# Kernel optimization log

Measured on AMD Instinct MI355X. Metric: run time of the kernel, lower is better.

Reference implementation:

```python
import jax, jax.numpy as jnp
import numpy as np

N, G, L, C = 32768, 128, 256, 128   # nodes, graphs, nodes-per-graph, channels
E, DS, DC, DR = 524288, 16, 4, 8    # edges, d_state, d_conv, dt_rank
EPS = 1e-5


def setup_inputs():
    key = jax.random.key(0)
    ks = jax.random.split(key, 16)
    s = 0.02
    p = lambda i, shape: jax.random.normal(ks[i], shape, jnp.float32) * s
    return {
        "x": jax.random.normal(ks[0], (N, C), jnp.float32),
        "edge_index": jax.random.randint(ks[1], (2, E), 0, N),
        "batch": jnp.repeat(jnp.arange(G), L),  # uniform graph sizes, sorted
        "gin_eps": jnp.float32(0.0),
        "gin_w1": p(2, (C, C)), "gin_b1": jnp.zeros((C,), jnp.float32),
        "gin_w2": p(3, (C, C)), "gin_b2": jnp.zeros((C,), jnp.float32),
        "in_proj_w": p(4, (2 * C, C)),
        "conv_w": p(5, (C, DC)), "conv_b": jnp.zeros((C,), jnp.float32),
        "x_proj_w": p(6, (DR + 2 * DS, C)),
        "dt_proj_w": p(7, (C, DR)),
        "dt_proj_b": jnp.full((C,), -4.0, jnp.float32),  # softplus -> small dt
        "A_log": jnp.log(jnp.broadcast_to(jnp.arange(1, DS + 1, dtype=jnp.float32), (C, DS))),
        "Dp": jnp.ones((C,), jnp.float32),
        "out_proj_w": p(8, (C, C)),
        "mlp_w1": p(9, (2 * C, C)), "mlp_b1": jnp.zeros((2 * C,), jnp.float32),
        "mlp_w2": p(10, (C, 2 * C)), "mlp_b2": jnp.zeros((C,), jnp.float32),
        "g1": jnp.ones((C,), jnp.float32), "be1": jnp.zeros((C,), jnp.float32),
        "g2": jnp.ones((C,), jnp.float32), "be2": jnp.zeros((C,), jnp.float32),
        "g3": jnp.ones((C,), jnp.float32), "be3": jnp.zeros((C,), jnp.float32),
    }


def batch_norm(h, g, b):
    # BatchNorm1d forward (batch statistics, biased var), eps=1e-5
    mu = h.mean(0)
    var = h.var(0)
    return (h - mu) * jax.lax.rsqrt(var + EPS) * g + b


def mamba(xd, in_proj_w, conv_w, conv_b, x_proj_w, dt_proj_w, dt_proj_b, A_log, Dp, out_proj_w):
    # xd: [G, L, C]; Mamba with expand=1 (d_inner == C)
    xz = jnp.einsum('glc,dc->gld', xd, in_proj_w)        # [G,L,2C]
    xs, z = jnp.split(xz, 2, axis=-1)
    # depthwise causal conv1d, kernel DC, left-pad DC-1
    xc = jax.lax.conv_general_dilated(
        xs.transpose(0, 2, 1), conv_w[:, None, :], (1,), [(DC - 1, 0)],
        dimension_numbers=('NCH', 'OIH', 'NCH'), feature_group_count=C)
    xs = jax.nn.silu(xc.transpose(0, 2, 1) + conv_b)     # [G,L,C]
    xdbl = jnp.einsum('gld,ed->gle', xs, x_proj_w)       # [G,L,DR+2*DS]
    dtr, Bm, Cm = jnp.split(xdbl, [DR, DR + DS], axis=-1)
    dt = jax.nn.softplus(jnp.einsum('glr,dr->gld', dtr, dt_proj_w) + dt_proj_b)  # [G,L,C]
    A = -jnp.exp(A_log)                                   # [C,DS]

    def step(hst, t):
        dt_t, B_t, C_t, x_t = t                           # [G,C],[G,DS],[G,DS],[G,C]
        dA = jnp.exp(dt_t[..., None] * A)                 # [G,C,DS]
        hst = dA * hst + dt_t[..., None] * B_t[:, None, :] * x_t[..., None]
        return hst, (hst * C_t[:, None, :]).sum(-1)       # y_t: [G,C]

    h0 = jnp.zeros((G, C, DS), xd.dtype)
    _, y = jax.lax.scan(step, h0, (dt.transpose(1, 0, 2), Bm.transpose(1, 0, 2),
                                   Cm.transpose(1, 0, 2), xs.transpose(1, 0, 2)))
    y = y.transpose(1, 0, 2) + Dp * xs                    # [G,L,C]
    y = y * jax.nn.silu(z)
    return jnp.einsum('gld,cd->glc', y, out_proj_w)


def _forward(edge_index, x, gin_eps, gin_w1, gin_b1, gin_w2, gin_b2,
             in_proj_w, conv_w, conv_b, x_proj_w, dt_proj_w, dt_proj_b,
             A_log, Dp, out_proj_w, mlp_w1, mlp_b1, mlp_w2, mlp_b2,
             g1, be1, g2, be2, g3, be3):
    # --- local MPNN branch: GIN conv + residual + norm1 (dropout=0, eval) ---
    agg = jax.ops.segment_sum(x[edge_index[0]], edge_index[1], num_segments=N)
    hg = (1.0 + gin_eps) * x + agg
    hg = jax.nn.relu(hg @ gin_w1.T + gin_b1) @ gin_w2.T + gin_b2
    h1 = batch_norm(hg + x, g1, be1)
    # --- Mamba branch over dense batch (uniform sizes -> reshape, mask all-true) ---
    xd = x.reshape(G, L, C)
    hm = mamba(xd, in_proj_w, conv_w, conv_b, x_proj_w, dt_proj_w, dt_proj_b,
               A_log, Dp, out_proj_w).reshape(N, C)
    h2 = batch_norm(hm + x, g2, be2)
    # --- combine + MLP + norm3 ---
    out = h1 + h2
    out = out + (jax.nn.relu(out @ mlp_w1.T + mlp_b1) @ mlp_w2.T + mlp_b2)
    out = batch_norm(out, g3, be3)
    return out, h2


def reference(x, edge_index, batch, gin_eps, gin_w1, gin_b1, gin_w2, gin_b2,
              in_proj_w, conv_w, conv_b, x_proj_w, dt_proj_w, dt_proj_b,
              A_log, Dp, out_proj_w, mlp_w1, mlp_b1, mlp_w2, mlp_b2,
              g1, be1, g2, be2, g3, be3):
    del batch  # uniform graph sizes encoded in (G, L)
    return _forward(edge_index, x, gin_eps, gin_w1, gin_b1, gin_w2, gin_b2,
                    in_proj_w, conv_w, conv_b, x_proj_w, dt_proj_w, dt_proj_b,
                    A_log, Dp, out_proj_w, mlp_w1, mlp_b1, mlp_w2, mlp_b2,
                    g1, be1, g2, be2, g3, be3)
```

## Files before the change

kernel.cpp:

```cpp
#include <hip/hip_runtime.h>
#include <hip/hip_bf16.h>

#define NN 32768
#define GG 128
#define LL 256
#define CC 128
#define EE 524288
#define NCHUNK 8
#define TCH 32

typedef __attribute__((ext_vector_type(8))) short short8v;
typedef __attribute__((ext_vector_type(4))) short short4v;
typedef __attribute__((ext_vector_type(4))) float floatx4;

__device__ inline short f2bf(float f) {
    __hip_bfloat16 h = __float2bfloat16(f);
    short s; __builtin_memcpy(&s, &h, 2); return s;
}
__device__ inline float b2f(unsigned short u) {
    unsigned v = ((unsigned)u) << 16; float f; __builtin_memcpy(&f, &v, 4); return f;
}
__device__ inline floatx4 mfma16(short8v a, short8v b, floatx4 c) {
    return __builtin_amdgcn_mfma_f32_16x16x32_bf16(a, b, c, 0, 0, 0);
}
__device__ inline float softplus_f(float v) {
    return (v > 20.f) ? v : __logf(1.f + __expf(v));
}

__global__ __launch_bounds__(256)
void wprep_kernel(const float* __restrict__ gw1, const float* __restrict__ gw2,
                  const float* __restrict__ ipw, const float* __restrict__ xpw,
                  const float* __restrict__ opw, const float* __restrict__ mw1,
                  const float* __restrict__ mw2, const float* __restrict__ dtw,
                  unsigned short* __restrict__ wb, int* __restrict__ cnt,
                  float* __restrict__ stats)
{
    int b = blockIdx.x, tid = threadIdx.x;
    if (b < 74) {
        const float* src; int dstoff, lb;
        if (b < 8)       { src = gw1;        dstoff = 0;      lb = b; }
        else if (b < 16) { src = gw2;        dstoff = 16384;  lb = b - 8; }
        else if (b < 32) { src = ipw;        dstoff = 32768;  lb = b - 16; }
        else if (b < 34) { src = xpw + 1024; dstoff = 81920;  lb = b - 32; }
        else if (b < 42) { src = opw;        dstoff = 86016;  lb = b - 34; }
        else if (b < 58) { src = mw1;        dstoff = 102400; lb = b - 42; }
        else             { src = mw2;        dstoff = 135168; lb = b - 58; }
        size_t i = (size_t)lb * 2048 + tid * 8;
        float4 a = *(const float4*)(src + i);
        float4 c = *(const float4*)(src + i + 4);
        short8v s = { f2bf(a.x), f2bf(a.y), f2bf(a.z), f2bf(a.w),
                      f2bf(c.x), f2bf(c.y), f2bf(c.z), f2bf(c.w) };
        *(short8v*)(wb + dstoff + i) = s;
    } else if (b < 138) {
        int i = (b - 74) * 256 + tid;
        int d = i >> 7, c = i & 127;
        float s = 0.f;
#pragma unroll
        for (int r = 0; r < 8; r++) s = fmaf(dtw[d * 8 + r], xpw[r * 128 + c], s);
        wb[65536 + i] = (unsigned short)f2bf(s);
    } else if (b < 170) {
        int idx = (b - 138) * 1024 + tid * 4;
        *(int4*)(cnt + idx) = make_int4(0, 0, 0, 0);
    } else {
        stats[tid] = 0.f; stats[256 + tid] = 0.f; stats[512 + tid] = 0.f;
    }
}

__global__ __launch_bounds__(256) void hist_kernel(const int* __restrict__ ei,
    int* __restrict__ cnt)
{
    int e = blockIdx.x * 256 + threadIdx.x;
    atomicAdd(&cnt[ei[EE + e]], 1);
}

__global__ __launch_bounds__(1024) void scan32k_kernel(const int* __restrict__ cnt,
    int* __restrict__ base, int* __restrict__ cursor)
{
    __shared__ int part[1024];
    int tid = threadIdx.x;
    int local[32];
    int s = 0;
#pragma unroll
    for (int j = 0; j < 32; j++) { local[j] = cnt[tid * 32 + j]; s += local[j]; }
    part[tid] = s;
    __syncthreads();
    for (int off = 1; off < 1024; off <<= 1) {
        int v = (tid >= off) ? part[tid - off] : 0;
        __syncthreads();
        part[tid] += v;
        __syncthreads();
    }
    int run = part[tid] - s;
#pragma unroll
    for (int j = 0; j < 32; j++) {
        base[tid * 32 + j] = run;
        cursor[tid * 32 + j] = run;
        run += local[j];
    }
    if (tid == 0) base[NN] = EE;
}

__global__ __launch_bounds__(256) void permute_kernel(const int* __restrict__ ei,
    int* __restrict__ cursor, int* __restrict__ perm)
{
    int e = blockIdx.x * 256 + threadIdx.x;
    int dst = ei[EE + e];
    int pos = atomicAdd(&cursor[dst], 1);
    perm[pos] = ei[e];
}

__global__ __launch_bounds__(256) void gather_kernel(const int* __restrict__ perm,
    const int* __restrict__ base, const unsigned short* __restrict__ xb,
    const float* __restrict__ epsp, unsigned short* __restrict__ hgin)
{
    int node = blockIdx.x * 8 + (threadIdx.x >> 5);
    int c4 = threadIdx.x & 31;
    int b0 = base[node], b1 = base[node + 1];
    float s0 = 0, s1 = 0, s2 = 0, s3 = 0;
    float t0 = 0, t1 = 0, t2 = 0, t3 = 0;
    int i = b0;
    for (; i + 1 < b1; i += 2) {
        short4v v0 = *(const short4v*)(xb + (size_t)perm[i] * CC + c4 * 4);
        short4v v1 = *(const short4v*)(xb + (size_t)perm[i + 1] * CC + c4 * 4);
        s0 += b2f((unsigned short)v0[0]); s1 += b2f((unsigned short)v0[1]);
        s2 += b2f((unsigned short)v0[2]); s3 += b2f((unsigned short)v0[3]);
        t0 += b2f((unsigned short)v1[0]); t1 += b2f((unsigned short)v1[1]);
        t2 += b2f((unsigned short)v1[2]); t3 += b2f((unsigned short)v1[3]);
    }
    if (i < b1) {
        short4v v0 = *(const short4v*)(xb + (size_t)perm[i] * CC + c4 * 4);
        s0 += b2f((unsigned short)v0[0]); s1 += b2f((unsigned short)v0[1]);
        s2 += b2f((unsigned short)v0[2]); s3 += b2f((unsigned short)v0[3]);
    }
    float e1 = 1.f + epsp[0];
    short4v xv = *(const short4v*)(xb + (size_t)node * CC + c4 * 4);
    float r0 = fmaf(e1, b2f((unsigned short)xv[0]), s0 + t0);
    float r1 = fmaf(e1, b2f((unsigned short)xv[1]), s1 + t1);
    float r2 = fmaf(e1, b2f((unsigned short)xv[2]), s2 + t2);
    float r3 = fmaf(e1, b2f((unsigned short)xv[3]), s3 + t3);
    short4v o = { f2bf(r0), f2bf(r1), f2bf(r2), f2bf(r3) };
    *(short4v*)(hgin + (size_t)node * CC + c4 * 4) = o;
}

__global__ __launch_bounds__(256) void xb_kernel(const float* __restrict__ x,
    unsigned short* __restrict__ xb)
{
    size_t i = (size_t)blockIdx.x * 256 + threadIdx.x;
    float4 a = *(const float4*)(x + i * 8);
    float4 b = *(const float4*)(x + i * 8 + 4);
    short8v s = { f2bf(a.x), f2bf(a.y), f2bf(a.z), f2bf(a.w),
                  f2bf(b.x), f2bf(b.y), f2bf(b.z), f2bf(b.w) };
    *(short8v*)(xb + i * 8) = s;
}

template<int K, int ACT, bool HAS_BIAS, int RESID, bool STATS, int OUTM>
__global__ __launch_bounds__(256)
void rgemm(const unsigned short* __restrict__ A,
           const unsigned short* __restrict__ Wb,
           const float* __restrict__ bias,
           const unsigned short* __restrict__ residb,
           float* out, float* out_b1,
           unsigned short* outb, unsigned short* outb_b1, int ldo,
           float* ssum, float* ssq)
{
    __shared__ float sred[256];
    const int tid = threadIdx.x;
    const int by = blockIdx.y;
    const int lane = tid & 63;
    const int wc = tid >> 6;
    const int rql = lane & 15;
    const int kseg = (lane >> 4) * 8;
    const int rsub = (lane >> 4) * 4;
    constexpr int NK = K / 32;

    if (STATS) sred[tid] = 0.f;

    int colg[2];
    colg[0] = by * 128 + wc * 32 + rql;
    colg[1] = colg[0] + 16;
    short8v w0[NK], w1[NK];
    {
        const unsigned short* wp0 = Wb + (size_t)colg[0] * K + kseg;
        const unsigned short* wp1 = Wb + (size_t)colg[1] * K + kseg;
#pragma unroll
        for (int kk = 0; kk < NK; kk++) {
            w0[kk] = *(const short8v*)(wp0 + kk * 32);
            w1[kk] = *(const short8v*)(wp1 + kk * 32);
        }
    }
    float bcol[2] = {0.f, 0.f};
    if (HAS_BIAS) { bcol[0] = bias[colg[0]]; bcol[1] = bias[colg[1]]; }
    float ssumr[2] = {0.f, 0.f}, ssqr[2] = {0.f, 0.f};

    short8v abuf[2][NK][2];
    {
        const unsigned short* ap = A + (size_t)(blockIdx.x * 32 + rql) * K + kseg;
#pragma unroll
        for (int kk = 0; kk < NK; kk++) {
            abuf[0][kk][0] = *(const short8v*)(ap + kk * 32);
            abuf[0][kk][1] = *(const short8v*)(ap + 16 * K + kk * 32);
        }
    }
    float* op = by ? out_b1 : out;
    unsigned short* opb = by ? outb_b1 : outb;

#pragma unroll
    for (int t = 0; t < 2; t++) {
        const int R0 = (blockIdx.x + t * 512) * 32;
        if (t == 0) {
            const unsigned short* ap = A + (size_t)((blockIdx.x + 512) * 32 + rql) * K + kseg;
#pragma unroll
            for (int kk = 0; kk < NK; kk++) {
                abuf[1][kk][0] = *(const short8v*)(ap + kk * 32);
                abuf[1][kk][1] = *(const short8v*)(ap + 16 * K + kk * 32);
            }
        }
        __builtin_amdgcn_sched_barrier(0);
        floatx4 acc[2][2];
#pragma unroll
        for (int m = 0; m < 2; m++)
#pragma unroll
            for (int n = 0; n < 2; n++)
#pragma unroll
                for (int r = 0; r < 4; r++) acc[m][n][r] = 0.f;
#pragma unroll
        for (int kk = 0; kk < NK; kk++) {
            acc[0][0] = mfma16(abuf[t][kk][0], w0[kk], acc[0][0]);
            acc[0][1] = mfma16(abuf[t][kk][0], w1[kk], acc[0][1]);
            acc[1][0] = mfma16(abuf[t][kk][1], w0[kk], acc[1][0]);
            acc[1][1] = mfma16(abuf[t][kk][1], w1[kk], acc[1][1]);
        }
#pragma unroll
        for (int m = 0; m < 2; m++) {
#pragma unroll
            for (int r = 0; r < 4; r++) {
                int row_g = R0 + m * 16 + rsub + r;
#pragma unroll
                for (int n = 0; n < 2; n++) {
                    float v = acc[m][n][r] + bcol[n];
                    if (ACT == 1) v = fmaxf(v, 0.f);
                    if (ACT == 2) v = softplus_f(v);
                    if (RESID == 1)
                        v += b2f(residb[(size_t)row_g * CC + colg[n]]);
                    int cl_ = colg[n] - by * 128;
                    if (OUTM & 1) op[(size_t)row_g * ldo + cl_] = v;
                    if (OUTM & 2) opb[(size_t)row_g * ldo + cl_] = (unsigned short)f2bf(v);
                    if (STATS) { ssumr[n] += v; ssqr[n] += v * v; }
                }
            }
        }
    }
    if (STATS) {
        __syncthreads();
#pragma unroll
        for (int n = 0; n < 2; n++) {
            int cl = wc * 32 + n * 16 + rql;
            atomicAdd(&sred[cl], ssumr[n]);
            atomicAdd(&sred[128 + cl], ssqr[n]);
        }
        __syncthreads();
        if (tid < 128) {
            atomicAdd(&ssum[tid], sred[tid]);
            atomicAdd(&ssq[tid], sred[128 + tid]);
        }
    }
}

template<int KMID>
__global__ __launch_bounds__(256)
void fused2(const unsigned short* __restrict__ A,
            const unsigned short* __restrict__ W1b, const float* __restrict__ b1,
            const unsigned short* __restrict__ W2b, const float* __restrict__ b2,
            const unsigned short* __restrict__ residb,
            float* __restrict__ outp,
            float* ssum, float* ssq)
{
    constexpr int NF1 = KMID / 64;
    constexpr int NK1 = 4;
    constexpr int NK2 = KMID / 32;
    constexpr int LDSW = KMID + 8;
    __shared__ unsigned short lds[2][32 * LDSW];
    __shared__ float sred[256];
    const int tid = threadIdx.x;
    const int lane = tid & 63;
    const int wc = tid >> 6;
    const int rql = lane & 15;
    const int kseg = (lane >> 4) * 8;
    const int rsub = (lane >> 4) * 4;

    sred[tid] = 0.f;

    short8v w1r[NF1][NK1];
    int colg1[NF1];
    float b1c[NF1];
#pragma unroll
    for (int f = 0; f < NF1; f++) {
        colg1[f] = wc * (16 * NF1) + f * 16 + rql;
        const unsigned short* wp = W1b + (size_t)colg1[f] * 128 + kseg;
#pragma unroll
        for (int kk = 0; kk < NK1; kk++) w1r[f][kk] = *(const short8v*)(wp + kk * 32);
        b1c[f] = b1[colg1[f]];
    }
    int colg2[2];
    colg2[0] = wc * 32 + rql;
    colg2[1] = colg2[0] + 16;
    float b2c[2] = { b2[colg2[0]], b2[colg2[1]] };
    float ssumr[2] = {0.f, 0.f}, ssqr[2] = {0.f, 0.f};

    short8v abuf[2][NK1][2];
    {
        const unsigned short* ap = A + (size_t)(blockIdx.x * 32 + rql) * 128 + kseg;
#pragma unroll
        for (int kk = 0; kk < NK1; kk++) {
            abuf[0][kk][0] = *(const short8v*)(ap + kk * 32);
            abuf[0][kk][1] = *(const short8v*)(ap + 16 * 128 + kk * 32);
        }
    }
    __syncthreads();

#pragma unroll
    for (int t = 0; t < 2; t++) {
        const int R0 = (blockIdx.x + t * 512) * 32;
        floatx4 acc1[2][NF1];
#pragma unroll
        for (int m = 0; m < 2; m++)
#pragma unroll
            for (int f = 0; f < NF1; f++)
#pragma unroll
                for (int r = 0; r < 4; r++) acc1[m][f][r] = 0.f;
#pragma unroll
        for (int kk = 0; kk < NK1; kk++)
#pragma unroll
            for (int m = 0; m < 2; m++)
#pragma unroll
                for (int f = 0; f < NF1; f++)
                    acc1[m][f] = mfma16(abuf[t][kk][m], w1r[f][kk], acc1[m][f]);
        unsigned short* L = &lds[t][0];
#pragma unroll
        for (int m = 0; m < 2; m++)
#pragma unroll
            for (int f = 0; f < NF1; f++)
#pragma unroll
                for (int r = 0; r < 4; r++) {
                    float v = fmaxf(acc1[m][f][r] + b1c[f], 0.f);
                    L[(m * 16 + rsub + r) * LDSW + colg1[f]] = (unsigned short)f2bf(v);
                }
        __syncthreads();
        if (t == 0) {
            const unsigned short* ap = A + (size_t)((blockIdx.x + 512) * 32 + rql) * 128 + kseg;
#pragma unroll
            for (int kk = 0; kk < NK1; kk++) {
                abuf[1][kk][0] = *(const short8v*)(ap + kk * 32);
                abuf[1][kk][1] = *(const short8v*)(ap + 16 * 128 + kk * 32);
            }
        }
        short8v w2a[NK2], w2b[NK2];
        {
            const unsigned short* wq0 = W2b + (size_t)colg2[0] * KMID + kseg;
            const unsigned short* wq1 = W2b + (size_t)colg2[1] * KMID + kseg;
#pragma unroll
            for (int kk = 0; kk < NK2; kk++) {
                w2a[kk] = *(const short8v*)(wq0 + kk * 32);
                w2b[kk] = *(const short8v*)(wq1 + kk * 32);
            }
        }
        floatx4 acc2[2][2];
#pragma unroll
        for (int m = 0; m < 2; m++)
#pragma unroll
            for (int n = 0; n < 2; n++)
#pragma unroll
                for (int r = 0; r < 4; r++) acc2[m][n][r] = 0.f;
#pragma unroll
        for (int kk = 0; kk < NK2; kk++) {
            short8v a2lo = *(const short8v*)&L[rql * LDSW + kseg + kk * 32];
            short8v a2hi = *(const short8v*)&L[(rql + 16) * LDSW + kseg + kk * 32];
            acc2[0][0] = mfma16(a2lo, w2a[kk], acc2[0][0]);
            acc2[0][1] = mfma16(a2lo, w2b[kk], acc2[0][1]);
            acc2[1][0] = mfma16(a2hi, w2a[kk], acc2[1][0]);
            acc2[1][1] = mfma16(a2hi, w2b[kk], acc2[1][1]);
        }
#pragma unroll
        for (int m = 0; m < 2; m++) {
#pragma unroll
            for (int r = 0; r < 4; r++) {
                int row_g = R0 + m * 16 + rsub + r;
#pragma unroll
                for (int n = 0; n < 2; n++) {
                    float v = acc2[m][n][r] + b2c[n];
                    v += b2f(residb[(size_t)row_g * CC + colg2[n]]);
                    outp[(size_t)row_g * CC + colg2[n]] = v;
                    ssumr[n] += v; ssqr[n] += v * v;
                }
            }
        }
    }
    __syncthreads();
#pragma unroll
    for (int n = 0; n < 2; n++) {
        atomicAdd(&sred[colg2[n]], ssumr[n]);
        atomicAdd(&sred[128 + colg2[n]], ssqr[n]);
    }
    __syncthreads();
    if (tid < 128) {
        atomicAdd(&ssum[tid], sred[tid]);
        atomicAdd(&ssq[tid], sred[128 + tid]);
    }
}

__global__ __launch_bounds__(256)
void mamba_front(const unsigned short* __restrict__ xb,
                 const unsigned short* __restrict__ ipwb,
                 const float* __restrict__ cw, const float* __restrict__ cb,
                 const unsigned short* __restrict__ wdtb, const float* __restrict__ dtbv,
                 const unsigned short* __restrict__ xpwb,
                 unsigned short* __restrict__ xsb, unsigned short* __restrict__ zb,
                 unsigned short* __restrict__ dtout, float* __restrict__ BCout)
{
    __shared__ unsigned short xsL[48 * 136];
    __shared__ unsigned short xcL[32 * 136];
    const int tid = threadIdx.x;
    const int lane = tid & 63;
    const int wv = tid >> 6;
    const int rql = lane & 15;
    const int kseg = (lane >> 4) * 8;
    const int rsub = (lane >> 4) * 4;
    const int R0 = blockIdx.x * 32;
    const int RB = R0 - 16;

    int coln[4];
#pragma unroll
    for (int n = 0; n < 4; n++) coln[n] = wv * 64 + n * 16 + rql;
    short8v wr[4][4];
#pragma unroll
    for (int n = 0; n < 4; n++) {
        const unsigned short* wp = ipwb + (size_t)coln[n] * 128 + kseg;
#pragma unroll
        for (int kk = 0; kk < 4; kk++) wr[n][kk] = *(const short8v*)(wp + kk * 32);
    }
    int arow[3];
#pragma unroll
    for (int m = 0; m < 3; m++) {
        int r = RB + m * 16 + rql;
        arow[m] = r < 0 ? 0 : r;
    }
    floatx4 acc[3][4];
#pragma unroll
    for (int m = 0; m < 3; m++)
#pragma unroll
        for (int n = 0; n < 4; n++)
#pragma unroll
            for (int r = 0; r < 4; r++) acc[m][n][r] = 0.f;
#pragma unroll
    for (int kb = 0; kb < 4; kb += 2) {
        short8v a2[3][2];
#pragma unroll
        for (int m = 0; m < 3; m++)
#pragma unroll
            for (int j = 0; j < 2; j++)
                a2[m][j] = *(const short8v*)(xb + (size_t)arow[m] * 128 + kseg + (kb + j) * 32);
        __builtin_amdgcn_sched_barrier(0);
#pragma unroll
        for (int j = 0; j < 2; j++)
#pragma unroll
            for (int m = 0; m < 3; m++)
#pragma unroll
                for (int n = 0; n < 4; n++)
                    acc[m][n] = mfma16(a2[m][j], wr[n][kb + j], acc[m][n]);
    }
    if (wv < 2) {
#pragma unroll
        for (int m = 0; m < 3; m++)
#pragma unroll
            for (int r = 0; r < 4; r++) {
                int row_l = m * 16 + rsub + r;
#pragma unroll
                for (int n = 0; n < 4; n++)
                    xsL[row_l * 136 + coln[n]] = (unsigned short)f2bf(acc[m][n][r]);
            }
    } else {
#pragma unroll
        for (int m = 1; m < 3; m++)
#pragma unroll
            for (int r = 0; r < 4; r++) {
                int row_g = RB + m * 16 + rsub + r;
#pragma unroll
                for (int n = 0; n < 4; n++)
                    zb[(size_t)row_g * 128 + (coln[n] - 128)] = (unsigned short)f2bf(acc[m][n][r]);
            }
    }
    __syncthreads();

    {
        int r = tid >> 3;
        int c0 = (tid & 7) * 16;
        int l = (R0 + r) & (LL - 1);
        const unsigned short* basep = &xsL[(16 + r) * 136 + c0];
        unsigned short o16[16];
#pragma unroll
        for (int half = 0; half < 2; half++) {
            short8v x0 = *(const short8v*)(basep + half * 8);
            short8v x1 = *(const short8v*)(basep - 136 + half * 8);
            short8v x2 = *(const short8v*)(basep - 272 + half * 8);
            short8v x3 = *(const short8v*)(basep - 408 + half * 8);
#pragma unroll
            for (int j = 0; j < 8; j++) {
                int c = c0 + half * 8 + j;
                float4 w = *(const float4*)(cw + c * 4);
                float v = cb[c];
                v = fmaf(b2f((unsigned short)x0[j]), w.w, v);
                if (l >= 1) v = fmaf(b2f((unsigned short)x1[j]), w.z, v);
                if (l >= 2) v = fmaf(b2f((unsigned short)x2[j]), w.y, v);
                if (l >= 3) v = fmaf(b2f((unsigned short)x3[j]), w.x, v);
                v = v / (1.f + __expf(-v));
                o16[half * 8 + j] = (unsigned short)f2bf(v);
            }
        }
#pragma unroll
        for (int half = 0; half < 2; half++) {
            short8v s;
#pragma unroll
            for (int j = 0; j < 8; j++) s[j] = (short)o16[half * 8 + j];
            *(short8v*)&xcL[r * 136 + c0 + half * 8] = s;
            *(short8v*)(xsb + (size_t)(R0 + r) * 128 + c0 + half * 8) = s;
        }
    }
    __syncthreads();

    int cold0 = wv * 32 + rql, cold1 = cold0 + 16;
    short8v wd0[4], wd1[4];
    {
        const unsigned short* wp0 = wdtb + (size_t)cold0 * 128 + kseg;
        const unsigned short* wp1 = wdtb + (size_t)cold1 * 128 + kseg;
#pragma unroll
        for (int kk = 0; kk < 4; kk++) {
            wd0[kk] = *(const short8v*)(wp0 + kk * 32);
            wd1[kk] = *(const short8v*)(wp1 + kk * 32);
        }
    }
    float bd0 = dtbv[cold0], bd1 = dtbv[cold1];
    int colb = wv * 16 + rql;
    short8v wbc[4];
    if (wv < 2) {
        const unsigned short* wp = xpwb + (size_t)colb * 128 + kseg;
#pragma unroll
        for (int kk = 0; kk < 4; kk++) wbc[kk] = *(const short8v*)(wp + kk * 32);
    }
    short8v a0[4], a1[4];
#pragma unroll
    for (int kk = 0; kk < 4; kk++) {
        a0[kk] = *(const short8v*)&xcL[rql * 136 + kseg + kk * 32];
        a1[kk] = *(const short8v*)&xcL[(16 + rql) * 136 + kseg + kk * 32];
    }
    floatx4 accd[2][2], accb[2];
#pragma unroll
    for (int m = 0; m < 2; m++) {
#pragma unroll
        for (int n = 0; n < 2; n++)
#pragma unroll
            for (int r = 0; r < 4; r++) accd[m][n][r] = 0.f;
#pragma unroll
        for (int r = 0; r < 4; r++) accb[m][r] = 0.f;
    }
#pragma unroll
    for (int kk = 0; kk < 4; kk++) {
        accd[0][0] = mfma16(a0[kk], wd0[kk], accd[0][0]);
        accd[0][1] = mfma16(a0[kk], wd1[kk], accd[0][1]);
        accd[1][0] = mfma16(a1[kk], wd0[kk], accd[1][0]);
        accd[1][1] = mfma16(a1[kk], wd1[kk], accd[1][1]);
        if (wv < 2) {
            accb[0] = mfma16(a0[kk], wbc[kk], accb[0]);
            accb[1] = mfma16(a1[kk], wbc[kk], accb[1]);
        }
    }
#pragma unroll
    for (int m = 0; m < 2; m++) {
#pragma unroll
        for (int r = 0; r < 4; r++) {
            int row_g = R0 + m * 16 + rsub + r;
            float v0 = softplus_f(accd[m][0][r] + bd0);
            float v1 = softplus_f(accd[m][1][r] + bd1);
            dtout[(size_t)row_g * 128 + cold0] = (unsigned short)f2bf(v0);
            dtout[(size_t)row_g * 128 + cold1] = (unsigned short)f2bf(v1);
            if (wv < 2) BCout[(size_t)row_g * 32 + colb] = accb[m][r];
        }
    }
}

__global__ __launch_bounds__(256) void scan_part_kernel(const float* __restrict__ BCp,
    const unsigned short* __restrict__ dtp, const unsigned short* __restrict__ xsp_,
    const float* __restrict__ Alog, float* __restrict__ Q, float* __restrict__ SDT)
{
    __shared__ float Bs[TCH * 16];
    __shared__ float dts[TCH * 64];
    __shared__ float xss[TCH * 64];
    int b = blockIdx.x;
    int g = b >> 4, ch = (b >> 3) & 1, chunk = b & 7;
    int t0 = chunk * TCH;
    int tid = threadIdx.x;
    for (int i4 = tid; i4 < TCH * 4; i4 += 256) {
        int t = i4 >> 2, j4 = i4 & 3;
        *(float4*)&Bs[t * 16 + j4 * 4] =
            *(const float4*)(BCp + (size_t)(g * LL + t0 + t) * 32 + j4 * 4);
    }
    for (int i4 = tid; i4 < TCH * 16; i4 += 256) {
        int t = i4 >> 4, c4 = i4 & 15;
        size_t off = (size_t)(g * LL + t0 + t) * CC + ch * 64 + c4 * 4;
        short4v dv = *(const short4v*)(dtp + off);
        short4v xv = *(const short4v*)(xsp_ + off);
        *(float4*)&dts[t * 64 + c4 * 4] = make_float4(
            b2f((unsigned short)dv[0]), b2f((unsigned short)dv[1]),
            b2f((unsigned short)dv[2]), b2f((unsigned short)dv[3]));
        *(float4*)&xss[t * 64 + c4 * 4] = make_float4(
            b2f((unsigned short)xv[0]), b2f((unsigned short)xv[1]),
            b2f((unsigned short)xv[2]), b2f((unsigned short)xv[3]));
    }
    int cl = tid >> 2, sp = tid & 3;
    int c = ch * 64 + cl;
    float ae[4];
#pragma unroll
    for (int j = 0; j < 4; j++) ae[j] = -__expf(Alog[c * 16 + sp * 4 + j]);
    __syncthreads();
    float q0 = 0, q1 = 0, q2 = 0, q3 = 0, sdt = 0;
    for (int t = TCH - 1; t >= 0; --t) {
        float dtv = dts[t * 64 + cl];
        float xv  = xss[t * 64 + cl];
        float u = dtv * xv;
        const float* bs = Bs + t * 16 + sp * 4;
        q0 = fmaf(__expf(ae[0] * sdt) * u, bs[0], q0);
        q1 = fmaf(__expf(ae[1] * sdt) * u, bs[1], q1);
        q2 = fmaf(__expf(ae[2] * sdt) * u, bs[2], q2);
        q3 = fmaf(__expf(ae[3] * sdt) * u, bs[3], q3);
        sdt += dtv;
    }
    float4* qp = (float4*)(Q + (((size_t)g * NCHUNK + chunk) * CC + c) * 16 + sp * 4);
    *qp = make_float4(q0, q1, q2, q3);
    if (sp == 0) SDT[((size_t)g * NCHUNK + chunk) * CC + c] = sdt;
}

__global__ __launch_bounds__(256) void scan_combine_kernel(const float* __restrict__ Q,
    const float* __restrict__ SDT, const float* __restrict__ Alog, float* __restrict__ Hin)
{
    int idx = blockIdx.x * 256 + threadIdx.x;
    int g = idx >> 11;
    int cs = idx & 2047;
    float ae = -__expf(Alog[cs]);
    float h = 0.f;
#pragma unroll
    for (int k = 0; k < NCHUNK; k++) {
        size_t o = ((size_t)g * NCHUNK + k);
        Hin[o * 2048 + cs] = h;
        float sdt = SDT[o * CC + (cs >> 4)];
        h = fmaf(__expf(ae * sdt), h, Q[o * 2048 + cs]);
    }
}

__global__ __launch_bounds__(256) void scan_final_kernel(const float* __restrict__ BCp,
    const unsigned short* __restrict__ dtp, const unsigned short* __restrict__ xsp_,
    const unsigned short* __restrict__ zb, const float* __restrict__ Alog,
    const float* __restrict__ Dp, const float* __restrict__ Hin,
    unsigned short* __restrict__ y2b)
{
    __shared__ float BCs[TCH * 32];
    __shared__ float dts[TCH * 64];
    __shared__ float xss[TCH * 64];
    int b = blockIdx.x;
    int g = b >> 4, ch = (b >> 3) & 1, chunk = b & 7;
    int t0 = chunk * TCH;
    int tid = threadIdx.x;
    for (int i4 = tid; i4 < TCH * 8; i4 += 256) {
        int t = i4 >> 3, j4 = i4 & 7;
        *(float4*)&BCs[t * 32 + j4 * 4] =
            *(const float4*)(BCp + (size_t)(g * LL + t0 + t) * 32 + j4 * 4);
    }
    for (int i4 = tid; i4 < TCH * 16; i4 += 256) {
        int t = i4 >> 4, c4 = i4 & 15;
        size_t off = (size_t)(g * LL + t0 + t) * CC + ch * 64 + c4 * 4;
        short4v dv = *(const short4v*)(dtp + off);
        short4v xv = *(const short4v*)(xsp_ + off);
        *(float4*)&dts[t * 64 + c4 * 4] = make_float4(
            b2f((unsigned short)dv[0]), b2f((unsigned short)dv[1]),
            b2f((unsigned short)dv[2]), b2f((unsigned short)dv[3]));
        *(float4*)&xss[t * 64 + c4 * 4] = make_float4(
            b2f((unsigned short)xv[0]), b2f((unsigned short)xv[1]),
            b2f((unsigned short)xv[2]), b2f((unsigned short)xv[3]));
    }
    int cl = tid >> 2, sp = tid & 3;
    int c = ch * 64 + cl;
    float ae[4];
#pragma unroll
    for (int j = 0; j < 4; j++) ae[j] = -__expf(Alog[c * 16 + sp * 4 + j]);
    float dpc = Dp[c];
    float4 hv = *(const float4*)(Hin + ((size_t)g * NCHUNK + chunk) * 2048 + c * 16 + sp * 4);
    float h0 = hv.x, h1 = hv.y, h2 = hv.z, h3 = hv.w;
    __syncthreads();
    const unsigned short* zg = zb + (size_t)(g * LL + t0) * CC + c;
    unsigned short* yg = y2b + (size_t)(g * LL + t0) * CC + c;
    for (int t = 0; t < TCH; t++) {
        float dtv = dts[t * 64 + cl];
        float xv  = xss[t * 64 + cl];
        float u = dtv * xv;
        const float* bc = BCs + t * 32 + sp * 4;
        h0 = fmaf(__expf(dtv * ae[0]), h0, u * bc[0]);
        h1 = fmaf(__expf(dtv * ae[1]), h1, u * bc[1]);
        h2 = fmaf(__expf(dtv * ae[2]), h2, u * bc[2]);
        h3 = fmaf(__expf(dtv * ae[3]), h3, u * bc[3]);
        float y = h0 * bc[16] + h1 * bc[17] + h2 * bc[18] + h3 * bc[19];
        y += __shfl_xor(y, 1);
        y += __shfl_xor(y, 2);
        if (sp == 0) {
            float zv = b2f(zg[t * CC]);
            float yo = fmaf(dpc, xv, y);
            yg[t * CC] = (unsigned short)f2bf(yo * (zv / (1.f + __expf(-zv))));
        }
    }
}

__global__ __launch_bounds__(256) void norm12_kernel(const float* __restrict__ p1,
    const float* __restrict__ p2, const float* __restrict__ stats,
    const float* g1, const float* be1, const float* g2, const float* be2,
    float* __restrict__ h2out, unsigned short* __restrict__ out12b)
{
    __shared__ float sc[512];
    int tid = threadIdx.x;
    if (tid < 128) {
        int c = tid;
        const float inv = 1.0f / NN;
        float m1 = stats[c] * inv;
        float v1 = fmaxf(stats[128 + c] * inv - m1 * m1, 0.f);
        float i1 = rsqrtf(v1 + 1e-5f);
        sc[c] = g1[c] * i1; sc[128 + c] = be1[c] - m1 * g1[c] * i1;
        float m2 = stats[256 + c] * inv;
        float v2 = fmaxf(stats[384 + c] * inv - m2 * m2, 0.f);
        float i2 = rsqrtf(v2 + 1e-5f);
        sc[256 + c] = g2[c] * i2; sc[384 + c] = be2[c] - m2 * g2[c] * i2;
    }
    __syncthreads();
    size_t idx = (size_t)blockIdx.x * 256 + tid;
    int c4 = (int)(idx & 31);
    float4 s1 = *(float4*)&sc[c4 * 4];
    float4 t1 = *(float4*)&sc[128 + c4 * 4];
    float4 s2 = *(float4*)&sc[256 + c4 * 4];
    float4 t2 = *(float4*)&sc[384 + c4 * 4];
    float4 a = *(const float4*)(p1 + idx * 4);
    float4 b = *(const float4*)(p2 + idx * 4);
    float4 h, o;
    h.x = fmaf(b.x, s2.x, t2.x); o.x = fmaf(a.x, s1.x, t1.x) + h.x;
    h.y = fmaf(b.y, s2.y, t2.y); o.y = fmaf(a.y, s1.y, t1.y) + h.y;
    h.z = fmaf(b.z, s2.z, t2.z); o.z = fmaf(a.z, s1.z, t1.z) + h.z;
    h.w = fmaf(b.w, s2.w, t2.w); o.w = fmaf(a.w, s1.w, t1.w) + h.w;
    *(float4*)(h2out + idx * 4) = h;
    short4v ob = { f2bf(o.x), f2bf(o.y), f2bf(o.z), f2bf(o.w) };
    *(short4v*)(out12b + idx * 4) = ob;
}

__global__ __launch_bounds__(256) void norm3_kernel(const float* __restrict__ p3,
    const float* __restrict__ stats, const float* g3, const float* be3,
    float* __restrict__ outp)
{
    __shared__ float sc[256];
    int tid = threadIdx.x;
    if (tid < 128) {
        int c = tid;
        const float inv = 1.0f / NN;
        float m = stats[512 + c] * inv;
        float v = fmaxf(stats[640 + c] * inv - m * m, 0.f);
        float iv = rsqrtf(v + 1e-5f);
        sc[c] = g3[c] * iv; sc[128 + c] = be3[c] - m * g3[c] * iv;
    }
    __syncthreads();
    size_t idx = (size_t)blockIdx.x * 256 + tid;
    int c4 = (int)(idx & 31);
    float4 s = *(float4*)&sc[c4 * 4];
    float4 t = *(float4*)&sc[128 + c4 * 4];
    float4 a = *(const float4*)(p3 + idx * 4);
    float4 o;
    o.x = fmaf(a.x, s.x, t.x); o.y = fmaf(a.y, s.y, t.y);
    o.z = fmaf(a.z, s.z, t.z); o.w = fmaf(a.w, s.w, t.w);
    *(float4*)(outp + idx * 4) = o;
}

extern "C" void kernel_launch(void* const* d_in, const int* in_sizes, int n_in,
                              void* d_out, int out_size, void* d_ws, size_t ws_size,
                              hipStream_t stream)
{
    (void)in_sizes; (void)n_in; (void)out_size; (void)ws_size;
    const float* x    = (const float*)d_in[0];
    const int*   ei   = (const int*)d_in[1];
    const float* eps  = (const float*)d_in[3];
    const float* gw1  = (const float*)d_in[4];
    const float* gb1  = (const float*)d_in[5];
    const float* gw2  = (const float*)d_in[6];
    const float* gb2  = (const float*)d_in[7];
    const float* ipw  = (const float*)d_in[8];
    const float* cw   = (const float*)d_in[9];
    const float* cb   = (const float*)d_in[10];
    const float* xpw  = (const float*)d_in[11];
    const float* dtw  = (const float*)d_in[12];
    const float* dtb  = (const float*)d_in[13];
    const float* Alog = (const float*)d_in[14];
    const float* Dp   = (const float*)d_in[15];
    const float* opw  = (const float*)d_in[16];
    const float* mw1  = (const float*)d_in[17];
    const float* mb1  = (const float*)d_in[18];
    const float* mw2  = (const float*)d_in[19];
    const float* mb2  = (const float*)d_in[20];
    const float* g1   = (const float*)d_in[21];
    const float* be1  = (const float*)d_in[22];
    const float* g2   = (const float*)d_in[23];
    const float* be2  = (const float*)d_in[24];
    const float* g3   = (const float*)d_in[25];
    const float* be3  = (const float*)d_in[26];

    float* outp = (float*)d_out;
    float* h2o  = outp + (size_t)NN * CC;
    float* p1 = outp;
    float* p2 = h2o;

    const size_t M1 = 1u << 20;
    float* ws = (float*)d_ws;
    float*  scr4   = ws;
    float*  BC     = ws + 4 * M1;
    unsigned short* zb      = (unsigned short*)(ws + 7 * M1);
    unsigned short* dtb_buf = (unsigned short*)(ws + 9 * M1);
    unsigned short* xb      = (unsigned short*)(ws + 11 * M1);
    unsigned short* hgin    = (unsigned short*)(ws + 13 * M1);
    unsigned short* xsb     = (unsigned short*)(ws + 15 * M1);
    unsigned short* out12b  = (unsigned short*)(ws + 17 * M1);
    float*  stats  = ws + 19 * M1;
    int*    cnt    = (int*)(stats + 768);
    int*    baseA  = cnt + NN;
    int*    cursor = baseA + NN + 1;
    int*    perm   = cursor + NN;
    float*  SDT    = (float*)(perm + EE);
    unsigned short* wbase = (unsigned short*)(SDT + 131072);
    unsigned short* gw1b = wbase;
    unsigned short* gw2b = wbase + 16384;
    unsigned short* ipwb = wbase + 32768;
    unsigned short* wdtb = wbase + 65536;
    unsigned short* xpwb = wbase + 81920;
    unsigned short* opwb = wbase + 86016;
    unsigned short* mw1b = wbase + 102400;
    unsigned short* mw2b = wbase + 135168;

    float* Qbuf = scr4;
    float* Hin  = scr4 + 2 * M1;
    float* p3   = scr4;
    unsigned short* y2b = hgin;

    wprep_kernel<<<dim3(171), 256, 0, stream>>>(gw1, gw2, ipw, xpw, opw, mw1, mw2,
                                                dtw, wbase, cnt, stats);
    xb_kernel<<<dim3(NN * CC / 8 / 256), 256, 0, stream>>>(x, xb);

    hist_kernel<<<dim3(EE / 256), 256, 0, stream>>>(ei, cnt);
    scan32k_kernel<<<dim3(1), 1024, 0, stream>>>(cnt, baseA, cursor);
    permute_kernel<<<dim3(EE / 256), 256, 0, stream>>>(ei, cursor, perm);
    gather_kernel<<<dim3(NN / 8), 256, 0, stream>>>(perm, baseA, xb, eps, hgin);

    fused2<128><<<dim3(512), 256, 0, stream>>>(
        hgin, gw1b, gb1, gw2b, gb2, xb, p1, stats + 0, stats + 128);

    mamba_front<<<dim3(NN / 32), 256, 0, stream>>>(
        xb, ipwb, cw, cb, wdtb, dtb, xpwb, xsb, zb, dtb_buf, BC);

    scan_part_kernel<<<dim3(GG * 16), 256, 0, stream>>>(BC, dtb_buf, xsb, Alog, Qbuf, SDT);
    scan_combine_kernel<<<dim3(GG * 2048 / 256), 256, 0, stream>>>(Qbuf, SDT, Alog, Hin);
    scan_final_kernel<<<dim3(GG * 16), 256, 0, stream>>>(BC, dtb_buf, xsb, zb, Alog, Dp, Hin, y2b);

    rgemm<128, 0, false, 1, true, 1><<<dim3(512, 1), 256, 0, stream>>>(
        y2b, opwb, nullptr, xb, p2, nullptr, nullptr, nullptr, 128, stats + 256, stats + 384);

    norm12_kernel<<<dim3(NN * CC / 4 / 256), 256, 0, stream>>>(
        p1, p2, stats, g1, be1, g2, be2, h2o, out12b);

    fused2<256><<<dim3(512), 256, 0, stream>>>(
        out12b, mw1b, mb1, mw2b, mb2, out12b, p3, stats + 512, stats + 640);

    norm3_kernel<<<dim3(NN * CC / 4 / 256), 256, 0, stream>>>(p3, stats, g3, be3, outp);
}
```

Before: 291.1 us.

## Fuse chunk scan partials into mamba_front and out_proj GEMM into scan output

```diff
diff --git a/kernel.cpp b/kernel.cpp
--- a/kernel.cpp
+++ b/kernel.cpp
@@ -153,119 +153,6 @@
     *(short8v*)(xb + i * 8) = s;
 }
 
-template<int K, int ACT, bool HAS_BIAS, int RESID, bool STATS, int OUTM>
-__global__ __launch_bounds__(256)
-void rgemm(const unsigned short* __restrict__ A,
-           const unsigned short* __restrict__ Wb,
-           const float* __restrict__ bias,
-           const unsigned short* __restrict__ residb,
-           float* out, float* out_b1,
-           unsigned short* outb, unsigned short* outb_b1, int ldo,
-           float* ssum, float* ssq)
-{
-    __shared__ float sred[256];
-    const int tid = threadIdx.x;
-    const int by = blockIdx.y;
-    const int lane = tid & 63;
-    const int wc = tid >> 6;
-    const int rql = lane & 15;
-    const int kseg = (lane >> 4) * 8;
-    const int rsub = (lane >> 4) * 4;
-    constexpr int NK = K / 32;
-
-    if (STATS) sred[tid] = 0.f;
-
-    int colg[2];
-    colg[0] = by * 128 + wc * 32 + rql;
-    colg[1] = colg[0] + 16;
-    short8v w0[NK], w1[NK];
-    {
-        const unsigned short* wp0 = Wb + (size_t)colg[0] * K + kseg;
-        const unsigned short* wp1 = Wb + (size_t)colg[1] * K + kseg;
-#pragma unroll
-        for (int kk = 0; kk < NK; kk++) {
-            w0[kk] = *(const short8v*)(wp0 + kk * 32);
-            w1[kk] = *(const short8v*)(wp1 + kk * 32);
-        }
-    }
-    float bcol[2] = {0.f, 0.f};
-    if (HAS_BIAS) { bcol[0] = bias[colg[0]]; bcol[1] = bias[colg[1]]; }
-    float ssumr[2] = {0.f, 0.f}, ssqr[2] = {0.f, 0.f};
-
-    short8v abuf[2][NK][2];
-    {
-        const unsigned short* ap = A + (size_t)(blockIdx.x * 32 + rql) * K + kseg;
-#pragma unroll
-        for (int kk = 0; kk < NK; kk++) {
-            abuf[0][kk][0] = *(const short8v*)(ap + kk * 32);
-            abuf[0][kk][1] = *(const short8v*)(ap + 16 * K + kk * 32);
-        }
-    }
-    float* op = by ? out_b1 : out;
-    unsigned short* opb = by ? outb_b1 : outb;
-
-#pragma unroll
-    for (int t = 0; t < 2; t++) {
-        const int R0 = (blockIdx.x + t * 512) * 32;
-        if (t == 0) {
-            const unsigned short* ap = A + (size_t)((blockIdx.x + 512) * 32 + rql) * K + kseg;
-#pragma unroll
-            for (int kk = 0; kk < NK; kk++) {
-                abuf[1][kk][0] = *(const short8v*)(ap + kk * 32);
-                abuf[1][kk][1] = *(const short8v*)(ap + 16 * K + kk * 32);
-            }
-        }
-        __builtin_amdgcn_sched_barrier(0);
-        floatx4 acc[2][2];
-#pragma unroll
-        for (int m = 0; m < 2; m++)
-#pragma unroll
-            for (int n = 0; n < 2; n++)
-#pragma unroll
-                for (int r = 0; r < 4; r++) acc[m][n][r] = 0.f;
-#pragma unroll
-        for (int kk = 0; kk < NK; kk++) {
-            acc[0][0] = mfma16(abuf[t][kk][0], w0[kk], acc[0][0]);
-            acc[0][1] = mfma16(abuf[t][kk][0], w1[kk], acc[0][1]);
-            acc[1][0] = mfma16(abuf[t][kk][1], w0[kk], acc[1][0]);
-            acc[1][1] = mfma16(abuf[t][kk][1], w1[kk], acc[1][1]);
-        }
-#pragma unroll
-        for (int m = 0; m < 2; m++) {
-#pragma unroll
-            for (int r = 0; r < 4; r++) {
-                int row_g = R0 + m * 16 + rsub + r;
-#pragma unroll
-                for (int n = 0; n < 2; n++) {
-                    float v = acc[m][n][r] + bcol[n];
-                    if (ACT == 1) v = fmaxf(v, 0.f);
-                    if (ACT == 2) v = softplus_f(v);
-                    if (RESID == 1)
-                        v += b2f(residb[(size_t)row_g * CC + colg[n]]);
-                    int cl_ = colg[n] - by * 128;
-                    if (OUTM & 1) op[(size_t)row_g * ldo + cl_] = v;
-                    if (OUTM & 2) opb[(size_t)row_g * ldo + cl_] = (unsigned short)f2bf(v);
-                    if (STATS) { ssumr[n] += v; ssqr[n] += v * v; }
-                }
-            }
-        }
-    }
-    if (STATS) {
-        __syncthreads();
-#pragma unroll
-        for (int n = 0; n < 2; n++) {
-            int cl = wc * 32 + n * 16 + rql;
-            atomicAdd(&sred[cl], ssumr[n]);
-            atomicAdd(&sred[128 + cl], ssqr[n]);
-        }
-        __syncthreads();
-        if (tid < 128) {
-            atomicAdd(&ssum[tid], sred[tid]);
-            atomicAdd(&ssq[tid], sred[128 + tid]);
-        }
-    }
-}
-
 template<int KMID>
 __global__ __launch_bounds__(256)
 void fused2(const unsigned short* __restrict__ A,
@@ -414,11 +301,14 @@
                  const float* __restrict__ cw, const float* __restrict__ cb,
                  const unsigned short* __restrict__ wdtb, const float* __restrict__ dtbv,
                  const unsigned short* __restrict__ xpwb,
+                 const float* __restrict__ Alog,
                  unsigned short* __restrict__ xsb, unsigned short* __restrict__ zb,
-                 unsigned short* __restrict__ dtout, float* __restrict__ BCout)
+                 unsigned short* __restrict__ dtout, float* __restrict__ BCout,
+                 float* __restrict__ Q, float* __restrict__ SDT)
 {
     __shared__ unsigned short xsL[48 * 136];
     __shared__ unsigned short xcL[32 * 136];
+    __shared__ float BsL[TCH * 16];
     const int tid = threadIdx.x;
     const int lane = tid & 63;
     const int wv = tid >> 6;
@@ -427,6 +317,8 @@
     const int rsub = (lane >> 4) * 4;
     const int R0 = blockIdx.x * 32;
     const int RB = R0 - 16;
+    const int g = blockIdx.x >> 3;
+    const int chunk = blockIdx.x & 7;
 
     int coln[4];
 #pragma unroll
@@ -527,6 +419,7 @@
     }
     __syncthreads();
 
+    unsigned short* dtL = xsL;
     int cold0 = wv * 32 + rql, cold1 = cold0 + 16;
     short8v wd0[4], wd1[4];
     {
@@ -577,65 +470,46 @@
     for (int m = 0; m < 2; m++) {
 #pragma unroll
         for (int r = 0; r < 4; r++) {
-            int row_g = R0 + m * 16 + rsub + r;
+            int tl = m * 16 + rsub + r;
+            int row_g = R0 + tl;
             float v0 = softplus_f(accd[m][0][r] + bd0);
             float v1 = softplus_f(accd[m][1][r] + bd1);
-            dtout[(size_t)row_g * 128 + cold0] = (unsigned short)f2bf(v0);
-            dtout[(size_t)row_g * 128 + cold1] = (unsigned short)f2bf(v1);
-            if (wv < 2) BCout[(size_t)row_g * 32 + colb] = accb[m][r];
-        }
-    }
-}
-
-__global__ __launch_bounds__(256) void scan_part_kernel(const float* __restrict__ BCp,
-    const unsigned short* __restrict__ dtp, const unsigned short* __restrict__ xsp_,
-    const float* __restrict__ Alog, float* __restrict__ Q, float* __restrict__ SDT)
-{
-    __shared__ float Bs[TCH * 16];
-    __shared__ float dts[TCH * 64];
-    __shared__ float xss[TCH * 64];
-    int b = blockIdx.x;
-    int g = b >> 4, ch = (b >> 3) & 1, chunk = b & 7;
-    int t0 = chunk * TCH;
-    int tid = threadIdx.x;
-    for (int i4 = tid; i4 < TCH * 4; i4 += 256) {
-        int t = i4 >> 2, j4 = i4 & 3;
-        *(float4*)&Bs[t * 16 + j4 * 4] =
-            *(const float4*)(BCp + (size_t)(g * LL + t0 + t) * 32 + j4 * 4);
-    }
-    for (int i4 = tid; i4 < TCH * 16; i4 += 256) {
-        int t = i4 >> 4, c4 = i4 & 15;
-        size_t off = (size_t)(g * LL + t0 + t) * CC + ch * 64 + c4 * 4;
-        short4v dv = *(const short4v*)(dtp + off);
-        short4v xv = *(const short4v*)(xsp_ + off);
-        *(float4*)&dts[t * 64 + c4 * 4] = make_float4(
-            b2f((unsigned short)dv[0]), b2f((unsigned short)dv[1]),
-            b2f((unsigned short)dv[2]), b2f((unsigned short)dv[3]));
-        *(float4*)&xss[t * 64 + c4 * 4] = make_float4(
-            b2f((unsigned short)xv[0]), b2f((unsigned short)xv[1]),
-            b2f((unsigned short)xv[2]), b2f((unsigned short)xv[3]));
-    }
-    int cl = tid >> 2, sp = tid & 3;
-    int c = ch * 64 + cl;
-    float ae[4];
-#pragma unroll
-    for (int j = 0; j < 4; j++) ae[j] = -__expf(Alog[c * 16 + sp * 4 + j]);
-    __syncthreads();
-    float q0 = 0, q1 = 0, q2 = 0, q3 = 0, sdt = 0;
-    for (int t = TCH - 1; t >= 0; --t) {
-        float dtv = dts[t * 64 + cl];
-        float xv  = xss[t * 64 + cl];
-        float u = dtv * xv;
-        const float* bs = Bs + t * 16 + sp * 4;
-        q0 = fmaf(__expf(ae[0] * sdt) * u, bs[0], q0);
-        q1 = fmaf(__expf(ae[1] * sdt) * u, bs[1], q1);
-        q2 = fmaf(__expf(ae[2] * sdt) * u, bs[2], q2);
-        q3 = fmaf(__expf(ae[3] * sdt) * u, bs[3], q3);
-        sdt += dtv;
-    }
-    float4* qp = (float4*)(Q + (((size_t)g * NCHUNK + chunk) * CC + c) * 16 + sp * 4);
-    *qp = make_float4(q0, q1, q2, q3);
-    if (sp == 0) SDT[((size_t)g * NCHUNK + chunk) * CC + c] = sdt;
+            unsigned short u0 = (unsigned short)f2bf(v0);
+            unsigned short u1 = (unsigned short)f2bf(v1);
+            dtout[(size_t)row_g * 128 + cold0] = u0;
+            dtout[(size_t)row_g * 128 + cold1] = u1;
+            dtL[tl * 136 + cold0] = u0;
+            dtL[tl * 136 + cold1] = u1;
+            if (wv < 2) {
+                BCout[(size_t)row_g * 32 + colb] = accb[m][r];
+                if (wv == 0) BsL[tl * 16 + colb] = accb[m][r];
+            }
+        }
+    }
+    __syncthreads();
+
+    for (int u = tid; u < 512; u += 256) {
+        int c = u >> 2, sp = u & 3;
+        float ae0 = -__expf(Alog[c * 16 + sp * 4 + 0]);
+        float ae1 = -__expf(Alog[c * 16 + sp * 4 + 1]);
+        float ae2 = -__expf(Alog[c * 16 + sp * 4 + 2]);
+        float ae3 = -__expf(Alog[c * 16 + sp * 4 + 3]);
+        float q0 = 0, q1 = 0, q2 = 0, q3 = 0, sdt = 0;
+        for (int t = TCH - 1; t >= 0; --t) {
+            float dtv = b2f(dtL[t * 136 + c]);
+            float xv  = b2f(xcL[t * 136 + c]);
+            float uu = dtv * xv;
+            const float* bs = &BsL[t * 16 + sp * 4];
+            q0 = fmaf(__expf(ae0 * sdt) * uu, bs[0], q0);
+            q1 = fmaf(__expf(ae1 * sdt) * uu, bs[1], q1);
+            q2 = fmaf(__expf(ae2 * sdt) * uu, bs[2], q2);
+            q3 = fmaf(__expf(ae3 * sdt) * uu, bs[3], q3);
+            sdt += dtv;
+        }
+        float4* qp = (float4*)(Q + (((size_t)g * NCHUNK + chunk) * CC + c) * 16 + sp * 4);
+        *qp = make_float4(q0, q1, q2, q3);
+        if (sp == 0) SDT[((size_t)g * NCHUNK + chunk) * CC + c] = sdt;
+    }
 }
 
 __global__ __launch_bounds__(256) void scan_combine_kernel(const float* __restrict__ Q,
@@ -655,64 +529,110 @@
     }
 }
 
-__global__ __launch_bounds__(256) void scan_final_kernel(const float* __restrict__ BCp,
+__global__ __launch_bounds__(512)
+void scan_out_kernel(const float* __restrict__ BCp,
     const unsigned short* __restrict__ dtp, const unsigned short* __restrict__ xsp_,
     const unsigned short* __restrict__ zb, const float* __restrict__ Alog,
     const float* __restrict__ Dp, const float* __restrict__ Hin,
-    unsigned short* __restrict__ y2b)
+    const unsigned short* __restrict__ opwb, const unsigned short* __restrict__ xb,
+    float* __restrict__ p2, float* ssum, float* ssq)
 {
     __shared__ float BCs[TCH * 32];
-    __shared__ float dts[TCH * 64];
-    __shared__ float xss[TCH * 64];
-    int b = blockIdx.x;
-    int g = b >> 4, ch = (b >> 3) & 1, chunk = b & 7;
-    int t0 = chunk * TCH;
-    int tid = threadIdx.x;
-    for (int i4 = tid; i4 < TCH * 8; i4 += 256) {
+    __shared__ unsigned short dts[TCH * 136];
+    __shared__ unsigned short xss[TCH * 136];
+    __shared__ unsigned short yL[TCH * 136];
+    __shared__ float sred[256];
+    const int b = blockIdx.x;
+    const int g = b >> 3, chunk = b & 7;
+    const int t0 = chunk * TCH;
+    const int tid = threadIdx.x;
+    if (tid < 256) sred[tid] = 0.f;
+    for (int i4 = tid; i4 < TCH * 8; i4 += 512) {
         int t = i4 >> 3, j4 = i4 & 7;
         *(float4*)&BCs[t * 32 + j4 * 4] =
             *(const float4*)(BCp + (size_t)(g * LL + t0 + t) * 32 + j4 * 4);
     }
-    for (int i4 = tid; i4 < TCH * 16; i4 += 256) {
-        int t = i4 >> 4, c4 = i4 & 15;
-        size_t off = (size_t)(g * LL + t0 + t) * CC + ch * 64 + c4 * 4;
-        short4v dv = *(const short4v*)(dtp + off);
-        short4v xv = *(const short4v*)(xsp_ + off);
-        *(float4*)&dts[t * 64 + c4 * 4] = make_float4(
-            b2f((unsigned short)dv[0]), b2f((unsigned short)dv[1]),
-            b2f((unsigned short)dv[2]), b2f((unsigned short)dv[3]));
-        *(float4*)&xss[t * 64 + c4 * 4] = make_float4(
-            b2f((unsigned short)xv[0]), b2f((unsigned short)xv[1]),
-            b2f((unsigned short)xv[2]), b2f((unsigned short)xv[3]));
-    }
-    int cl = tid >> 2, sp = tid & 3;
-    int c = ch * 64 + cl;
-    float ae[4];
-#pragma unroll
-    for (int j = 0; j < 4; j++) ae[j] = -__expf(Alog[c * 16 + sp * 4 + j]);
+    {
+        int t = tid >> 4, c8 = tid & 15;
+        size_t off = (size_t)(g * LL + t0 + t) * CC + c8 * 8;
+        *(short8v*)&dts[t * 136 + c8 * 8] = *(const short8v*)(dtp + off);
+        *(short8v*)&xss[t * 136 + c8 * 8] = *(const short8v*)(xsp_ + off);
+    }
+    const int c = tid >> 2, sp = tid & 3;
+    float ae0 = -__expf(Alog[c * 16 + sp * 4 + 0]);
+    float ae1 = -__expf(Alog[c * 16 + sp * 4 + 1]);
+    float ae2 = -__expf(Alog[c * 16 + sp * 4 + 2]);
+    float ae3 = -__expf(Alog[c * 16 + sp * 4 + 3]);
     float dpc = Dp[c];
     float4 hv = *(const float4*)(Hin + ((size_t)g * NCHUNK + chunk) * 2048 + c * 16 + sp * 4);
     float h0 = hv.x, h1 = hv.y, h2 = hv.z, h3 = hv.w;
     __syncthreads();
     const unsigned short* zg = zb + (size_t)(g * LL + t0) * CC + c;
-    unsigned short* yg = y2b + (size_t)(g * LL + t0) * CC + c;
     for (int t = 0; t < TCH; t++) {
-        float dtv = dts[t * 64 + cl];
-        float xv  = xss[t * 64 + cl];
+        float dtv = b2f(dts[t * 136 + c]);
+        float xv  = b2f(xss[t * 136 + c]);
         float u = dtv * xv;
-        const float* bc = BCs + t * 32 + sp * 4;
-        h0 = fmaf(__expf(dtv * ae[0]), h0, u * bc[0]);
-        h1 = fmaf(__expf(dtv * ae[1]), h1, u * bc[1]);
-        h2 = fmaf(__expf(dtv * ae[2]), h2, u * bc[2]);
-        h3 = fmaf(__expf(dtv * ae[3]), h3, u * bc[3]);
+        const float* bc = &BCs[t * 32 + sp * 4];
+        h0 = fmaf(__expf(dtv * ae0), h0, u * bc[0]);
+        h1 = fmaf(__expf(dtv * ae1), h1, u * bc[1]);
+        h2 = fmaf(__expf(dtv * ae2), h2, u * bc[2]);
+        h3 = fmaf(__expf(dtv * ae3), h3, u * bc[3]);
         float y = h0 * bc[16] + h1 * bc[17] + h2 * bc[18] + h3 * bc[19];
         y += __shfl_xor(y, 1);
         y += __shfl_xor(y, 2);
         if (sp == 0) {
             float zv = b2f(zg[t * CC]);
             float yo = fmaf(dpc, xv, y);
-            yg[t * CC] = (unsigned short)f2bf(yo * (zv / (1.f + __expf(-zv))));
-        }
+            yL[t * 136 + c] = (unsigned short)f2bf(yo * (zv / (1.f + __expf(-zv))));
+        }
+    }
+    __syncthreads();
+
+    const int lane = tid & 63;
+    const int wv = tid >> 6;
+    const int rql = lane & 15;
+    const int kseg = (lane >> 4) * 8;
+    const int rsub = (lane >> 4) * 4;
+    const int colg = wv * 16 + rql;
+    short8v w[4];
+    {
+        const unsigned short* wp = opwb + (size_t)colg * 128 + kseg;
+#pragma unroll
+        for (int kk = 0; kk < 4; kk++) w[kk] = *(const short8v*)(wp + kk * 32);
+    }
+    floatx4 acc[2];
+#pragma unroll
+    for (int m = 0; m < 2; m++)
+#pragma unroll
+        for (int r = 0; r < 4; r++) acc[m][r] = 0.f;
+#pragma unroll
+    for (int kk = 0; kk < 4; kk++) {
+        short8v alo = *(const short8v*)&yL[rql * 136 + kseg + kk * 32];
+        short8v ahi = *(const short8v*)&yL[(16 + rql) * 136 + kseg + kk * 32];
+        acc[0] = mfma16(alo, w[kk], acc[0]);
+        acc[1] = mfma16(ahi, w[kk], acc[1]);
+    }
+    float sumr = 0.f, sqr = 0.f;
+#pragma unroll
+    for (int m = 0; m < 2; m++) {
+#pragma unroll
+        for (int r = 0; r < 4; r++) {
+            int row_g = g * LL + t0 + m * 16 + rsub + r;
+            float v = acc[m][r] + b2f(xb[(size_t)row_g * CC + colg]);
+            p2[(size_t)row_g * CC + colg] = v;
+            sumr += v; sqr += v * v;
+        }
+    }
+    sumr += __shfl_xor(sumr, 16); sumr += __shfl_xor(sumr, 32);
+    sqr  += __shfl_xor(sqr, 16);  sqr  += __shfl_xor(sqr, 32);
+    if ((lane >> 4) == 0) {
+        atomicAdd(&sred[colg], sumr);
+        atomicAdd(&sred[128 + colg], sqr);
+    }
+    __syncthreads();
+    if (tid < 128) {
+        atomicAdd(&ssum[tid], sred[tid]);
+        atomicAdd(&ssq[tid], sred[128 + tid]);
     }
 }
 
@@ -846,7 +766,6 @@
     float* Qbuf = scr4;
     float* Hin  = scr4 + 2 * M1;
     float* p3   = scr4;
-    unsigned short* y2b = hgin;
 
     wprep_kernel<<<dim3(171), 256, 0, stream>>>(gw1, gw2, ipw, xpw, opw, mw1, mw2,
                                                 dtw, wbase, cnt, stats);
@@ -861,14 +780,12 @@
         hgin, gw1b, gb1, gw2b, gb2, xb, p1, stats + 0, stats + 128);
 
     mamba_front<<<dim3(NN / 32), 256, 0, stream>>>(
-        xb, ipwb, cw, cb, wdtb, dtb, xpwb, xsb, zb, dtb_buf, BC);
-
-    scan_part_kernel<<<dim3(GG * 16), 256, 0, stream>>>(BC, dtb_buf, xsb, Alog, Qbuf, SDT);
+        xb, ipwb, cw, cb, wdtb, dtb, xpwb, Alog, xsb, zb, dtb_buf, BC, Qbuf, SDT);
+
     scan_combine_kernel<<<dim3(GG * 2048 / 256), 256, 0, stream>>>(Qbuf, SDT, Alog, Hin);
-    scan_final_kernel<<<dim3(GG * 16), 256, 0, stream>>>(BC, dtb_buf, xsb, zb, Alog, Dp, Hin, y2b);
-
-    rgemm<128, 0, false, 1, true, 1><<<dim3(512, 1), 256, 0, stream>>>(
-        y2b, opwb, nullptr, xb, p2, nullptr, nullptr, nullptr, 128, stats + 256, stats + 384);
+
+    scan_out_kernel<<<dim3(GG * NCHUNK), 512, 0, stream>>>(
+        BC, dtb_buf, xsb, zb, Alog, Dp, Hin, opwb, xb, p2, stats + 256, stats + 384);
 
     norm12_kernel<<<dim3(NN * CC / 4 / 256), 256, 0, stream>>>(
         p1, p2, stats, g1, be1, g2, be2, h2o, out12b);
```

Result: faster. 279.0 us (-4.1%).
